# Optimization experiments

Measured on AMD Instinct MI355X. Metric: run time of the kernel, lower is better.

Reference implementation:

```python
import jax
jax.config.update("jax_enable_x64", True)
import jax.numpy as jnp
import numpy as np

B = 4            # batch size
Z, Y, X = 41, 1024, 1024   # spatial shape (all coords < 1025, matching the hash base)
NT = 2_000_000   # raw teacher voxels (with duplicates)
NS = 800_000     # student voxels (subset of teacher unique coords)
C = 32           # feature channels
M = 1025         # hash base from the original module


def _hash(idx):
    # idx: [N,4] int -> int64 scalar hash; batch in high bits so sorting the hash
    # == lexicographic sort by (batch, c1, c2, c3), matching torch.unique(dim=0).
    w = jnp.array([M ** 3, M ** 2, M, 1], dtype=jnp.int64)
    return idx.astype(jnp.int64) @ w


def setup_inputs() -> dict:
    rng = np.random.default_rng(0)
    b = rng.integers(0, B, NT)
    z = rng.integers(0, Z, NT)
    y = rng.integers(0, Y, NT)
    x = rng.integers(0, X, NT)
    teacher_indices = np.stack([b, z, y, x], axis=1).astype(np.int32)

    # student indices must be a subset of teacher's unique coords (forward asserts this)
    h = (b.astype(np.int64) * M ** 3 + z.astype(np.int64) * M ** 2
         + y.astype(np.int64) * M + x.astype(np.int64))
    _, first = np.unique(h, return_index=True)
    pick = rng.choice(first, size=NS, replace=False)
    student_indices = teacher_indices[pick]

    key = jax.random.key(0)
    teacher_features = jax.random.normal(key, (NT, C), dtype=jnp.float32)
    return {
        "teacher_features": teacher_features,
        "teacher_indices": jnp.asarray(teacher_indices),
        "student_indices": jnp.asarray(student_indices),
    }


def reference(teacher_features, teacher_indices, student_indices):
    n_t = teacher_indices.shape[0]
    FILL = jnp.int64(2 ** 62)  # padding hash, sorts to the end

    # --- bev_out_3d: unique(dim=0) + index_add_ dedup ---
    h_t = _hash(teacher_indices)
    uniq, first_idx, inv = jnp.unique(
        h_t, size=n_t, fill_value=FILL, return_index=True, return_inverse=True
    )
    feat_unique = jax.ops.segment_sum(teacher_features, inv, num_segments=n_t)

    # --- per-batch isin join + masked gather ---
    # Teacher unique rows are hash-sorted (== lex-sorted by batch, coords).
    # The matched subset, in teacher order, is exactly the sorted student hashes
    # (student is a subset of teacher unique), concatenated batch-by-batch ==
    # a single global sort since batch occupies the high bits.
    h_s = jnp.sort(_hash(student_indices))
    pos = jnp.searchsorted(uniq, h_s)          # [NS] positions into unique rows
    feat = feat_unique[pos]                    # [NS, C]
    indice = teacher_indices[first_idx[pos]]   # [NS, 4]
    return feat, indice
```

## Files before the change

kernel.cpp:

```cpp
#include <hip/hip_runtime.h>
#include <stdint.h>

typedef unsigned long long u64;
typedef u64 u64x2 __attribute__((ext_vector_type(2)));

#define NWORDS 2686976u
#define GW 4096u
#define NGROUPS 656u

struct __align__(16) Combo { u64 word; uint32_t prefix; uint32_t pad; };

__device__ __forceinline__ uint32_t pack4(int4 v) {
    return (((uint32_t)v.x * 41u + (uint32_t)v.y) << 20) |
           ((uint32_t)v.z << 10) | (uint32_t)v.w;
}

__global__ void set_bits(const int* __restrict__ sidx, Combo* __restrict__ combo, int ns) {
    int i = blockIdx.x * blockDim.x + threadIdx.x;
    if (i >= ns) return;
    uint32_t k = pack4(((const int4*)sidx)[i]);
    atomicOr(&combo[k >> 6].word, 1ull << (k & 63u));
}

__global__ void group_popcount(const Combo* __restrict__ combo, uint32_t* __restrict__ groupSum) {
    __shared__ uint32_t s[256];
    uint32_t t = 0;
    size_t base = (size_t)blockIdx.x * GW;
    #pragma unroll
    for (int j = 0; j < 16; ++j)
        t += (uint32_t)__popcll(combo[base + j * 256u + threadIdx.x].word);
    s[threadIdx.x] = t;
    __syncthreads();
    #pragma unroll
    for (int off = 128; off > 0; off >>= 1) {
        if (threadIdx.x < (unsigned)off) s[threadIdx.x] += s[threadIdx.x + off];
        __syncthreads();
    }
    if (threadIdx.x == 0) groupSum[blockIdx.x] = s[0];
}

__global__ void scan_groups(uint32_t* __restrict__ groupSum, int n) {
    __shared__ uint32_t s[256];
    uint32_t run = 0;
    for (int c = 0; c < n; c += 256) {
        int i = c + (int)threadIdx.x;
        uint32_t v = (i < n) ? groupSum[i] : 0u;
        s[threadIdx.x] = v;
        __syncthreads();
        #pragma unroll
        for (int off = 1; off < 256; off <<= 1) {
            uint32_t u = (threadIdx.x >= (unsigned)off) ? s[threadIdx.x - off] : 0u;
            __syncthreads();
            s[threadIdx.x] += u;
            __syncthreads();
        }
        if (i < n) groupSum[i] = s[threadIdx.x] - v + run;
        run += s[255];
        __syncthreads();
    }
}

__global__ void word_prefix_indice(Combo* __restrict__ combo,
                                   const uint32_t* __restrict__ groupBase,
                                   float* __restrict__ outI) {
    __shared__ uint32_t s[256];
    const int tid = threadIdx.x;
    size_t w0 = (size_t)blockIdx.x * GW + (size_t)tid * 16;
    u64 w[16];
    uint32_t tsum = 0;
    #pragma unroll
    for (int j = 0; j < 16; ++j) { w[j] = combo[w0 + j].word; tsum += (uint32_t)__popcll(w[j]); }
    s[tid] = tsum;
    __syncthreads();
    #pragma unroll
    for (int off = 1; off < 256; off <<= 1) {
        uint32_t u = (tid >= off) ? s[tid - off] : 0u;
        __syncthreads();
        s[tid] += u;
        __syncthreads();
    }
    uint32_t run = groupBase[blockIdx.x] + s[tid] - tsum;
    #pragma unroll
    for (int j = 0; j < 16; ++j) {
        u64x2 rec; rec.x = w[j]; rec.y = (u64)run;
        ((u64x2*)combo)[w0 + j] = rec;
        u64 word = w[j];
        uint32_t kw = (uint32_t)(w0 + j) << 6;
        while (word) {
            int b = (int)__builtin_ctzll(word);
            word &= word - 1;
            uint32_t k = kw | (uint32_t)b;
            uint32_t bz = k >> 20;
            ((float4*)outI)[run++] = make_float4(
                (float)(bz / 41u), (float)(bz % 41u),
                (float)((k >> 10) & 1023u), (float)(k & 1023u));
        }
    }
}

__global__ void teacher_probe(const int* __restrict__ tidx, const Combo* __restrict__ combo,
                              uint32_t* __restrict__ cnt, int* __restrict__ pos, int nt) {
    int t = blockIdx.x * blockDim.x + threadIdx.x;
    if (t >= nt) return;
    uint32_t k = pack4(((const int4*)tidx)[t]);
    u64x2 e = ((const u64x2*)combo)[k >> 6];
    u64 word = e.x;
    u64 bit  = 1ull << (k & 63u);
    if (word & bit) {
        int p = (int)((uint32_t)e.y + (uint32_t)__popcll(word & (bit - 1ull)));
        pos[t] = p;
        atomicAdd(&cnt[p], 1u);
    } else {
        pos[t] = -1;
    }
}

__global__ void zero_multi(const uint32_t* __restrict__ cnt, float* __restrict__ feat, int ns) {
    int s = blockIdx.x * blockDim.x + threadIdx.x;
    if (s >= ns) return;
    if (cnt[s] > 1u) {
        float4* d4 = (float4*)(feat + (size_t)s * 32);
        #pragma unroll
        for (int q = 0; q < 8; ++q) d4[q] = make_float4(0.f, 0.f, 0.f, 0.f);
    }
}

__global__ void teacher_write(const float* __restrict__ tfeat, const int* __restrict__ pos,
                              const uint32_t* __restrict__ cnt, float* __restrict__ feat, int nt) {
    int t = blockIdx.x * blockDim.x + threadIdx.x;
    if (t >= nt) return;
    int p = pos[t];
    if (p < 0) return;
    const float4* src = (const float4*)(tfeat + (size_t)t * 32);
    float* dst = feat + (size_t)p * 32;
    if (cnt[p] == 1u) {
        float4* d4 = (float4*)dst;
        #pragma unroll
        for (int q = 0; q < 8; ++q) d4[q] = src[q];
    } else {
        #pragma unroll
        for (int q = 0; q < 8; ++q) {
            float4 f = src[q];
            atomicAdd(dst + q * 4 + 0, f.x);
            atomicAdd(dst + q * 4 + 1, f.y);
            atomicAdd(dst + q * 4 + 2, f.z);
            atomicAdd(dst + q * 4 + 3, f.w);
        }
    }
}

extern "C" void kernel_launch(void* const* d_in, const int* in_sizes, int n_in,
                              void* d_out, int out_size, void* d_ws, size_t ws_size,
                              hipStream_t stream) {
    const float* tfeat = (const float*)d_in[0];
    const int*   tidx  = (const int*)d_in[1];
    const int*   sidx  = (const int*)d_in[2];

    const int NT = in_sizes[1] / 4;
    const int NS = in_sizes[2] / 4;

    float* feat = (float*)d_out;
    float* outI = (float*)d_out + (size_t)NS * 32;

    char* base = (char*)d_ws;
    Combo*    combo    = (Combo*)base;
    uint32_t* cnt      = (uint32_t*)(base + (size_t)NWORDS * sizeof(Combo));
    size_t    zeroBytes = (size_t)NWORDS * sizeof(Combo) + (size_t)NS * 4;
    uint32_t* groupSum = cnt + NS;
    int*      pos      = (int*)(groupSum + NGROUPS);

    hipMemsetAsync(d_ws, 0, zeroBytes, stream);

    set_bits<<<(NS + 255) / 256, 256, 0, stream>>>(sidx, combo, NS);
    group_popcount<<<NGROUPS, 256, 0, stream>>>(combo, groupSum);
    scan_groups<<<1, 256, 0, stream>>>(groupSum, NGROUPS);
    word_prefix_indice<<<NGROUPS, 256, 0, stream>>>(combo, groupSum, outI);
    teacher_probe<<<(NT + 255) / 256, 256, 0, stream>>>(tidx, combo, cnt, pos, NT);
    zero_multi<<<(NS + 255) / 256, 256, 0, stream>>>(cnt, feat, NS);
    teacher_write<<<(NT + 255) / 256, 256, 0, stream>>>(tfeat, pos, cnt, feat, NT);
}
```

Measured before the change: 228.8 us.

## Fuse group popcount and scan into single-pass decoupled prefix kernel

Replaces the three-kernel prefix pipeline (group popcount, single-block group scan, word prefix emit) with one kernel. Each block publishes its total via a release-store flag and then sums all predecessor totals with spin-waiting acquire loads, which removes two launches and a second pass over the bitmap. Separately, the teacher probe and write kernels now handle two voxels per thread to raise memory-level parallelism. The spin-wait relies on earlier blocks being scheduled first (656 blocks should be co-resident). Each block also rereads all predecessor flags rather than using a lookback chain, which costs quadratic reads.

```diff
diff --git a/kernel.cpp b/kernel.cpp
--- a/kernel.cpp
+++ b/kernel.cpp
@@ -22,54 +22,18 @@
     atomicOr(&combo[k >> 6].word, 1ull << (k & 63u));
 }
 
-__global__ void group_popcount(const Combo* __restrict__ combo, uint32_t* __restrict__ groupSum) {
+__global__ void prefix_emit(Combo* __restrict__ combo, u64* __restrict__ state,
+                            float* __restrict__ outI) {
     __shared__ uint32_t s[256];
-    uint32_t t = 0;
-    size_t base = (size_t)blockIdx.x * GW;
-    #pragma unroll
-    for (int j = 0; j < 16; ++j)
-        t += (uint32_t)__popcll(combo[base + j * 256u + threadIdx.x].word);
-    s[threadIdx.x] = t;
-    __syncthreads();
-    #pragma unroll
-    for (int off = 128; off > 0; off >>= 1) {
-        if (threadIdx.x < (unsigned)off) s[threadIdx.x] += s[threadIdx.x + off];
-        __syncthreads();
-    }
-    if (threadIdx.x == 0) groupSum[blockIdx.x] = s[0];
-}
+    __shared__ uint32_t baseSh;
+    const int tid = threadIdx.x, bid = blockIdx.x;
+    const size_t w0 = (size_t)bid * GW + (size_t)tid * 16;
 
-__global__ void scan_groups(uint32_t* __restrict__ groupSum, int n) {
-    __shared__ uint32_t s[256];
-    uint32_t run = 0;
-    for (int c = 0; c < n; c += 256) {
-        int i = c + (int)threadIdx.x;
-        uint32_t v = (i < n) ? groupSum[i] : 0u;
-        s[threadIdx.x] = v;
-        __syncthreads();
-        #pragma unroll
-        for (int off = 1; off < 256; off <<= 1) {
-            uint32_t u = (threadIdx.x >= (unsigned)off) ? s[threadIdx.x - off] : 0u;
-            __syncthreads();
-            s[threadIdx.x] += u;
-            __syncthreads();
-        }
-        if (i < n) groupSum[i] = s[threadIdx.x] - v + run;
-        run += s[255];
-        __syncthreads();
-    }
-}
-
-__global__ void word_prefix_indice(Combo* __restrict__ combo,
-                                   const uint32_t* __restrict__ groupBase,
-                                   float* __restrict__ outI) {
-    __shared__ uint32_t s[256];
-    const int tid = threadIdx.x;
-    size_t w0 = (size_t)blockIdx.x * GW + (size_t)tid * 16;
     u64 w[16];
     uint32_t tsum = 0;
     #pragma unroll
     for (int j = 0; j < 16; ++j) { w[j] = combo[w0 + j].word; tsum += (uint32_t)__popcll(w[j]); }
+
     s[tid] = tsum;
     __syncthreads();
     #pragma unroll
@@ -79,7 +43,29 @@
         s[tid] += u;
         __syncthreads();
     }
-    uint32_t run = groupBase[blockIdx.x] + s[tid] - tsum;
+    uint32_t exclInBlock = s[tid] - tsum;
+
+    if (tid == 0)
+        __hip_atomic_store(&state[bid], (1ull << 32) | (u64)s[255],
+                           __ATOMIC_RELEASE, __HIP_MEMORY_SCOPE_AGENT);
+
+    if (tid == 0) baseSh = 0u;
+    if (bid > 0 && tid < 64) {
+        uint32_t sum = 0;
+        for (int i = bid - 1 - tid; i >= 0; i -= 64) {
+            u64 st;
+            do {
+                st = __hip_atomic_load(&state[i], __ATOMIC_ACQUIRE, __HIP_MEMORY_SCOPE_AGENT);
+            } while ((st >> 32) == 0ull);
+            sum += (uint32_t)st;
+        }
+        #pragma unroll
+        for (int off = 32; off > 0; off >>= 1) sum += __shfl_down(sum, off);
+        if (tid == 0) baseSh = sum;
+    }
+    __syncthreads();
+    uint32_t run = baseSh + exclInBlock;
+
     #pragma unroll
     for (int j = 0; j < 16; ++j) {
         u64x2 rec; rec.x = w[j]; rec.y = (u64)run;
@@ -98,12 +84,7 @@
     }
 }
 
-__global__ void teacher_probe(const int* __restrict__ tidx, const Combo* __restrict__ combo,
-                              uint32_t* __restrict__ cnt, int* __restrict__ pos, int nt) {
-    int t = blockIdx.x * blockDim.x + threadIdx.x;
-    if (t >= nt) return;
-    uint32_t k = pack4(((const int4*)tidx)[t]);
-    u64x2 e = ((const u64x2*)combo)[k >> 6];
+__device__ __forceinline__ void probe_one(uint32_t k, u64x2 e, uint32_t* cnt, int* pos, int t) {
     u64 word = e.x;
     u64 bit  = 1ull << (k & 63u);
     if (word & bit) {
@@ -112,6 +93,23 @@
         atomicAdd(&cnt[p], 1u);
     } else {
         pos[t] = -1;
+    }
+}
+
+__global__ void teacher_probe(const int* __restrict__ tidx, const Combo* __restrict__ combo,
+                              uint32_t* __restrict__ cnt, int* __restrict__ pos, int nt) {
+    int i = blockIdx.x * blockDim.x + threadIdx.x;
+    int t0 = i * 2, t1 = i * 2 + 1;
+    if (t0 >= nt) return;
+    uint32_t k0 = pack4(((const int4*)tidx)[t0]);
+    u64x2 e0 = ((const u64x2*)combo)[k0 >> 6];
+    if (t1 < nt) {
+        uint32_t k1 = pack4(((const int4*)tidx)[t1]);
+        u64x2 e1 = ((const u64x2*)combo)[k1 >> 6];
+        probe_one(k0, e0, cnt, pos, t0);
+        probe_one(k1, e1, cnt, pos, t1);
+    } else {
+        probe_one(k0, e0, cnt, pos, t0);
     }
 }
 
@@ -125,12 +123,9 @@
     }
 }
 
-__global__ void teacher_write(const float* __restrict__ tfeat, const int* __restrict__ pos,
-                              const uint32_t* __restrict__ cnt, float* __restrict__ feat, int nt) {
-    int t = blockIdx.x * blockDim.x + threadIdx.x;
-    if (t >= nt) return;
-    int p = pos[t];
-    if (p < 0) return;
+__device__ __forceinline__ void write_one(const float* __restrict__ tfeat, int t, int p,
+                                          const uint32_t* __restrict__ cnt,
+                                          float* __restrict__ feat) {
     const float4* src = (const float4*)(tfeat + (size_t)t * 32);
     float* dst = feat + (size_t)p * 32;
     if (cnt[p] == 1u) {
@@ -149,6 +144,16 @@
     }
 }
 
+__global__ void teacher_write(const float* __restrict__ tfeat, const int* __restrict__ pos,
+                              const uint32_t* __restrict__ cnt, float* __restrict__ feat, int nt) {
+    int i = blockIdx.x * blockDim.x + threadIdx.x;
+    int t0 = i * 2, t1 = i * 2 + 1;
+    if (t0 >= nt) return;
+    int2 pp = (t1 < nt) ? *(const int2*)(pos + t0) : make_int2(pos[t0], -1);
+    if (pp.x >= 0) write_one(tfeat, t0, pp.x, cnt, feat);
+    if (pp.y >= 0) write_one(tfeat, t1, pp.y, cnt, feat);
+}
+
 extern "C" void kernel_launch(void* const* d_in, const int* in_sizes, int n_in,
                               void* d_out, int out_size, void* d_ws, size_t ws_size,
                               hipStream_t stream) {
@@ -163,19 +168,18 @@
     float* outI = (float*)d_out + (size_t)NS * 32;
 
     char* base = (char*)d_ws;
-    Combo*    combo    = (Combo*)base;
-    uint32_t* cnt      = (uint32_t*)(base + (size_t)NWORDS * sizeof(Combo));
-    size_t    zeroBytes = (size_t)NWORDS * sizeof(Combo) + (size_t)NS * 4;
-    uint32_t* groupSum = cnt + NS;
-    int*      pos      = (int*)(groupSum + NGROUPS);
+    Combo*    combo = (Combo*)base;
+    uint32_t* cnt   = (uint32_t*)(base + (size_t)NWORDS * sizeof(Combo));
+    u64*      state = (u64*)(cnt + NS);
+    int*      pos   = (int*)(state + NGROUPS);
+    size_t zeroBytes = (size_t)NWORDS * sizeof(Combo) + (size_t)NS * 4 + (size_t)NGROUPS * 8;
 
     hipMemsetAsync(d_ws, 0, zeroBytes, stream);
 
     set_bits<<<(NS + 255) / 256, 256, 0, stream>>>(sidx, combo, NS);
-    group_popcount<<<NGROUPS, 256, 0, stream>>>(combo, groupSum);
-    scan_groups<<<1, 256, 0, stream>>>(groupSum, NGROUPS);
-    word_prefix_indice<<<NGROUPS, 256, 0, stream>>>(combo, groupSum, outI);
-    teacher_probe<<<(NT + 255) / 256, 256, 0, stream>>>(tidx, combo, cnt, pos, NT);
+    prefix_emit<<<NGROUPS, 256, 0, stream>>>(combo, state, outI);
+    int halfT = (NT + 1) / 2;
+    teacher_probe<<<(halfT + 255) / 256, 256, 0, stream>>>(tidx, combo, cnt, pos, NT);
     zero_multi<<<(NS + 255) / 256, 256, 0, stream>>>(cnt, feat, NS);
-    teacher_write<<<(NT + 255) / 256, 256, 0, stream>>>(tfeat, pos, cnt, feat, NT);
+    teacher_write<<<(halfT + 255) / 256, 256, 0, stream>>>(tfeat, pos, cnt, feat, NT);
 }
```

New measurement: 288.8 us. +26.2%, slower.

## Fuse teacher probe and write with overflow list, fold group scan into prefix kernel

Applied to the files above, without the earlier changes.

The teacher probe and feature write are merged into one kernel. The first thread to claim a student slot copies its features directly, and later duplicates are appended to an overflow list that a small drain kernel sums in with atomics. This removes the pos array round-trip, the per-slot zeroing pass and the re-read of counts. The single-block group scan is also dropped: each prefix block sums the preceding group totals itself with a wave reduction, saving one serial launch. In exchange there is a global atomic counter for overflow entries and some redundant per-block summation.

```diff
diff --git a/kernel.cpp b/kernel.cpp
--- a/kernel.cpp
+++ b/kernel.cpp
@@ -39,33 +39,13 @@
     if (threadIdx.x == 0) groupSum[blockIdx.x] = s[0];
 }
 
-__global__ void scan_groups(uint32_t* __restrict__ groupSum, int n) {
-    __shared__ uint32_t s[256];
-    uint32_t run = 0;
-    for (int c = 0; c < n; c += 256) {
-        int i = c + (int)threadIdx.x;
-        uint32_t v = (i < n) ? groupSum[i] : 0u;
-        s[threadIdx.x] = v;
-        __syncthreads();
-        #pragma unroll
-        for (int off = 1; off < 256; off <<= 1) {
-            uint32_t u = (threadIdx.x >= (unsigned)off) ? s[threadIdx.x - off] : 0u;
-            __syncthreads();
-            s[threadIdx.x] += u;
-            __syncthreads();
-        }
-        if (i < n) groupSum[i] = s[threadIdx.x] - v + run;
-        run += s[255];
-        __syncthreads();
-    }
-}
-
 __global__ void word_prefix_indice(Combo* __restrict__ combo,
-                                   const uint32_t* __restrict__ groupBase,
+                                   const uint32_t* __restrict__ groupSum,
                                    float* __restrict__ outI) {
     __shared__ uint32_t s[256];
-    const int tid = threadIdx.x;
-    size_t w0 = (size_t)blockIdx.x * GW + (size_t)tid * 16;
+    __shared__ uint32_t baseSh;
+    const int tid = threadIdx.x, bid = blockIdx.x;
+    size_t w0 = (size_t)bid * GW + (size_t)tid * 16;
     u64 w[16];
     uint32_t tsum = 0;
     #pragma unroll
@@ -79,7 +59,16 @@
         s[tid] += u;
         __syncthreads();
     }
-    uint32_t run = groupBase[blockIdx.x] + s[tid] - tsum;
+    uint32_t exclInBlock = s[tid] - tsum;
+    if (tid < 64) {
+        uint32_t sum = 0;
+        for (int g = tid; g < bid; g += 64) sum += groupSum[g];
+        #pragma unroll
+        for (int off = 32; off > 0; off >>= 1) sum += __shfl_down(sum, off);
+        if (tid == 0) baseSh = sum;
+    }
+    __syncthreads();
+    uint32_t run = baseSh + exclInBlock;
     #pragma unroll
     for (int j = 0; j < 16; ++j) {
         u64x2 rec; rec.x = w[j]; rec.y = (u64)run;
@@ -98,46 +87,38 @@
     }
 }
 
-__global__ void teacher_probe(const int* __restrict__ tidx, const Combo* __restrict__ combo,
-                              uint32_t* __restrict__ cnt, int* __restrict__ pos, int nt) {
+__global__ void teacher_fused(const int* __restrict__ tidx, const float* __restrict__ tfeat,
+                              const Combo* __restrict__ combo, uint32_t* __restrict__ cnt,
+                              uint2* __restrict__ ovf, uint32_t* __restrict__ ovfCount,
+                              float* __restrict__ feat, int nt) {
     int t = blockIdx.x * blockDim.x + threadIdx.x;
     if (t >= nt) return;
     uint32_t k = pack4(((const int4*)tidx)[t]);
     u64x2 e = ((const u64x2*)combo)[k >> 6];
     u64 word = e.x;
     u64 bit  = 1ull << (k & 63u);
-    if (word & bit) {
-        int p = (int)((uint32_t)e.y + (uint32_t)__popcll(word & (bit - 1ull)));
-        pos[t] = p;
-        atomicAdd(&cnt[p], 1u);
+    if (!(word & bit)) return;
+    int p = (int)((uint32_t)e.y + (uint32_t)__popcll(word & (bit - 1ull)));
+    uint32_t old = atomicAdd(&cnt[p], 1u);
+    if (old == 0u) {
+        const float4* src = (const float4*)(tfeat + (size_t)t * 32);
+        float4* dst = (float4*)(feat + (size_t)p * 32);
+        #pragma unroll
+        for (int q = 0; q < 8; ++q) dst[q] = src[q];
     } else {
-        pos[t] = -1;
+        uint32_t idx = atomicAdd(ovfCount, 1u);
+        ovf[idx] = make_uint2((uint32_t)t, (uint32_t)p);
     }
 }
 
-__global__ void zero_multi(const uint32_t* __restrict__ cnt, float* __restrict__ feat, int ns) {
-    int s = blockIdx.x * blockDim.x + threadIdx.x;
-    if (s >= ns) return;
-    if (cnt[s] > 1u) {
-        float4* d4 = (float4*)(feat + (size_t)s * 32);
-        #pragma unroll
-        for (int q = 0; q < 8; ++q) d4[q] = make_float4(0.f, 0.f, 0.f, 0.f);
-    }
-}
-
-__global__ void teacher_write(const float* __restrict__ tfeat, const int* __restrict__ pos,
-                              const uint32_t* __restrict__ cnt, float* __restrict__ feat, int nt) {
-    int t = blockIdx.x * blockDim.x + threadIdx.x;
-    if (t >= nt) return;
-    int p = pos[t];
-    if (p < 0) return;
-    const float4* src = (const float4*)(tfeat + (size_t)t * 32);
-    float* dst = feat + (size_t)p * 32;
-    if (cnt[p] == 1u) {
-        float4* d4 = (float4*)dst;
-        #pragma unroll
-        for (int q = 0; q < 8; ++q) d4[q] = src[q];
-    } else {
+__global__ void drain_ovf(const float* __restrict__ tfeat, const uint2* __restrict__ ovf,
+                          const uint32_t* __restrict__ ovfCount, float* __restrict__ feat) {
+    uint32_t n = *ovfCount;
+    for (uint32_t i = blockIdx.x * blockDim.x + threadIdx.x; i < n;
+         i += gridDim.x * blockDim.x) {
+        uint2 e = ovf[i];
+        const float4* src = (const float4*)(tfeat + (size_t)e.x * 32);
+        float* dst = feat + (size_t)e.y * 32;
         #pragma unroll
         for (int q = 0; q < 8; ++q) {
             float4 f = src[q];
@@ -165,17 +146,17 @@
     char* base = (char*)d_ws;
     Combo*    combo    = (Combo*)base;
     uint32_t* cnt      = (uint32_t*)(base + (size_t)NWORDS * sizeof(Combo));
-    size_t    zeroBytes = (size_t)NWORDS * sizeof(Combo) + (size_t)NS * 4;
-    uint32_t* groupSum = cnt + NS;
-    int*      pos      = (int*)(groupSum + NGROUPS);
+    uint32_t* ovfCount = cnt + NS;
+    size_t    zeroBytes = (size_t)NWORDS * sizeof(Combo) + (size_t)NS * 4 + 8;
+    uint32_t* groupSum = ovfCount + 2;
+    uint2*    ovf      = (uint2*)(groupSum + NGROUPS);
 
     hipMemsetAsync(d_ws, 0, zeroBytes, stream);
 
     set_bits<<<(NS + 255) / 256, 256, 0, stream>>>(sidx, combo, NS);
     group_popcount<<<NGROUPS, 256, 0, stream>>>(combo, groupSum);
-    scan_groups<<<1, 256, 0, stream>>>(groupSum, NGROUPS);
     word_prefix_indice<<<NGROUPS, 256, 0, stream>>>(combo, groupSum, outI);
-    teacher_probe<<<(NT + 255) / 256, 256, 0, stream>>>(tidx, combo, cnt, pos, NT);
-    zero_multi<<<(NS + 255) / 256, 256, 0, stream>>>(cnt, feat, NS);
-    teacher_write<<<(NT + 255) / 256, 256, 0, stream>>>(tfeat, pos, cnt, feat, NT);
+    teacher_fused<<<(NT + 255) / 256, 256, 0, stream>>>(tidx, tfeat, combo, cnt,
+                                                        ovf, ovfCount, feat, NT);
+    drain_ovf<<<512, 256, 0, stream>>>(tfeat, ovf, ovfCount, feat);
 }
```

Measured after the change: 226.2 us. Within noise of the previous version (-1.2%).
